# Optimization experiments

Measured on AMD Instinct MI355X. Metric: run time of the kernel, lower is better.

## Reference

```python
import jax, jax.numpy as jnp
import numpy as np
from jax import lax

B, H, L, DK = 8, 8, 1024, 64
BN_EPS = 1e-5


def _conv_bn_sm(x, w, b, g, beta, pad):
    # x: [B, H, L] (N=batch, C=h heads as channels, spatial=L)
    y = lax.conv_general_dilated(x, w, (1,), [(pad, pad)], dimension_numbers=("NCH", "OIH", "NCH"))
    y = y + b[None, :, None]
    # BatchNorm1d in training mode: batch stats over (N, L) per channel, biased var
    mu = jnp.mean(y, axis=(0, 2), keepdims=True)
    var = jnp.var(y, axis=(0, 2), keepdims=True)
    y = (y - mu) * (g[None, :, None] / jnp.sqrt(var + BN_EPS)) + beta[None, :, None]
    return jax.nn.softmax(y, axis=-1)


def setup_inputs() -> dict:
    key = jax.random.key(0)
    ks = jax.random.split(key, 20)
    n = lambda i, shape, s=1.0: jax.random.normal(ks[i], shape, dtype=jnp.float32) * s
    inp = {
        "Q": n(0, (B, H, L, DK)),
        "K": n(1, (B, H, L, DK)),
        "V": n(2, (B, H, L, DK)),
        "attn_mask": jnp.ones((1,), dtype=bool),
        # proj_q / proj_k: Linear(d_k, 1, bias=False) weight [1, d_k] -> stored as [d_k]
        "wq": n(3, (DK,), 0.1), "wk": n(4, (DK,), 0.1),
        # proj_back_q / proj_back_k: Linear(1, d_k, bias=False) weight [d_k, 1] -> [d_k]
        "wbq": n(5, (DK,), 0.1), "wbk": n(6, (DK,), 0.1),
        # Conv1d(h, h, f) weights [out=h, in=h, f] + bias [h]
        "cq3_w": n(7, (H, H, 3), 0.2), "cq3_b": n(8, (H,), 0.05),
        "cq9_w": n(9, (H, H, 9), 0.1), "cq9_b": n(10, (H,), 0.05),
        "ck3_w": n(11, (H, H, 3), 0.2), "ck3_b": n(12, (H,), 0.05),
        "ck9_w": n(13, (H, H, 9), 0.1), "ck9_b": n(14, (H,), 0.05),
        # BatchNorm1d affine params
        "bnq3_g": jnp.ones((H,), jnp.float32), "bnq3_b": jnp.zeros((H,), jnp.float32),
        "bnq9_g": jnp.ones((H,), jnp.float32), "bnq9_b": jnp.zeros((H,), jnp.float32),
        "bnk3_g": jnp.ones((H,), jnp.float32), "bnk3_b": jnp.zeros((H,), jnp.float32),
        "bnk9_g": jnp.ones((H,), jnp.float32), "bnk9_b": jnp.zeros((H,), jnp.float32),
    }
    return inp


def reference(Q, K, V, attn_mask, wq, wk, wbq, wbk,
              cq3_w, cq3_b, cq9_w, cq9_b, ck3_w, ck3_b, ck9_w, ck9_b,
              bnq3_g, bnq3_b, bnq9_g, bnq9_b, bnk3_g, bnk3_b, bnk9_g, bnk9_b):
    b, h, l, d_k = Q.shape
    l_k = K.shape[2]
    # proj to scalar per position, reshape to [b, h, l]
    Qp = jnp.einsum("bhld,d->bhl", Q, wq)
    Kp = jnp.einsum("bhld,d->bhl", K, wk)
    # multi-scale conv + BN(train) + softmax branches
    q0 = _conv_bn_sm(Qp, cq3_w, cq3_b, bnq3_g, bnq3_b, 1)
    q1 = _conv_bn_sm(Qp, cq9_w, cq9_b, bnq9_g, bnq9_b, 4)
    k0 = _conv_bn_sm(Kp, ck3_w, ck3_b, bnk3_g, bnk3_b, 1)
    k1 = _conv_bn_sm(Kp, ck9_w, ck9_b, bnk9_g, bnk9_b, 4)
    # faithful to torch: cat along dim 0 then C-order reshape to [b,h,l,2], max over last
    Qm = jnp.max(jnp.concatenate([q0, q1], axis=0).reshape(b, h, l, 2), axis=-1)
    Km = jnp.max(jnp.concatenate([k0, k1], axis=0).reshape(b, h, l_k, 2), axis=-1)
    # proj back 1 -> d_k (no bias): outer with weight vector
    Qn = Qm[..., None] * wbq  # [b,h,l,d_k]
    Kn = Km[..., None] * wbk  # [b,h,l_k,d_k]
    scores = jnp.einsum("bhqd,bhkd->bhqk", Qn, Kn) / jnp.sqrt(jnp.float32(d_k))
    attn = jax.nn.softmax(scores, axis=-1)
    context = jnp.einsum("bhqk,bhkd->bhqd", attn, V)
    return (context, attn)
```

## Files before the change

kernel.cpp:

```cpp
#include <hip/hip_runtime.h>

constexpr int SL = 1024;
constexpr int NBH = 64;

constexpr int QP_OFF = 0;
constexpr int KP_OFF = 65536;
constexpr int Y_OFF  = 131072;
constexpr int P_OFF  = 393216;
constexpr int QM_OFF = 655360;
constexpr int KM_OFF = 720896;
constexpr int ST_OFF = 786432;
constexpr int C_OFF  = 786496;
constexpr int VT_OFF = 786560;

typedef __attribute__((ext_vector_type(8))) short short8;
typedef __attribute__((ext_vector_type(4))) float f32x4;

__device__ inline unsigned short f2bf(float x) {
    unsigned int u = __float_as_uint(x);
    unsigned int r = (u + 0x7fff + ((u >> 16) & 1)) >> 16;
    return (unsigned short)r;
}

__global__ __launch_bounds__(256) void k_proj(
    const float* __restrict__ Q, const float* __restrict__ K,
    const float* __restrict__ wq, const float* __restrict__ wk,
    const float* __restrict__ wbq, const float* __restrict__ wbk,
    float* __restrict__ ws)
{
    int wid  = (blockIdx.x * 256 + threadIdx.x) >> 6;
    int lane = threadIdx.x & 63;
    const int nrows = 2 * NBH * SL;
    if (wid < nrows) {
        bool isQ = wid < NBH * SL;
        int row = isQ ? wid : wid - NBH * SL;
        const float* src = isQ ? Q : K;
        const float* w   = isQ ? wq : wk;
        float v = src[row * 64 + lane] * w[lane];
        #pragma unroll
        for (int m = 32; m; m >>= 1) v += __shfl_xor(v, m);
        if (lane == 0) ws[(isQ ? QP_OFF : KP_OFF) + row] = v;
    } else if (wid == nrows) {
        float v = wbq[lane] * wbk[lane];
        #pragma unroll
        for (int m = 32; m; m >>= 1) v += __shfl_xor(v, m);
        if (lane == 0) ws[C_OFF] = v * 0.125f;
    }
}

__global__ __launch_bounds__(256) void k_conv(
    float* __restrict__ ws,
    const float* __restrict__ w0, const float* __restrict__ b0,
    const float* __restrict__ w1, const float* __restrict__ b1,
    const float* __restrict__ w2, const float* __restrict__ b2,
    const float* __restrict__ w3, const float* __restrict__ b3)
{
    int branch = blockIdx.x >> 6;
    int n = (blockIdx.x >> 3) & 7;
    int seg = blockIdx.x & 7;
    int t0 = seg * 128;
    const float* wp = branch == 0 ? w0 : branch == 1 ? w1 : branch == 2 ? w2 : w3;
    const float* bp = branch == 0 ? b0 : branch == 1 ? b1 : branch == 2 ? b2 : b3;
    const int F = (branch & 1) ? 9 : 3;
    const int PAD = F >> 1;
    const float* x = ws + ((branch < 2) ? QP_OFF : KP_OFF) + n * 8 * SL;

    __shared__ float xl[8][136];
    __shared__ float wl[8 * 8 * 9];
    __shared__ float bl[8];
    int tid = threadIdx.x;
    for (int i = tid; i < 8 * 8 * F; i += 256) wl[i] = wp[i];
    if (tid < 8) bl[tid] = bp[tid];
    for (int i = tid; i < 8 * 136; i += 256) {
        int ci = i >> 7;
        ci = i / 136; int tt = i - ci * 136;
        int ta = t0 + tt - 4;
        xl[ci][tt] = (ta >= 0 && ta < SL) ? x[ci * SL + ta] : 0.f;
    }
    __syncthreads();
    int c = tid >> 5, u = tid & 31;
    float s1 = 0.f, s2 = 0.f;
    float* yout = ws + Y_OFF + branch * (NBH * SL) + (n * 8 + c) * SL + t0;
    float res[4];
    #pragma unroll
    for (int q = 0; q < 4; q++) {
        int tl = u * 4 + q;
        float acc = bl[c];
        for (int ci = 0; ci < 8; ci++) {
            const float* xr = &xl[ci][tl + 4 - PAD];
            const float* wr = &wl[(c * 8 + ci) * F];
            for (int f = 0; f < F; f++) acc += wr[f] * xr[f];
        }
        res[q] = acc;
        s1 += acc; s2 += acc * acc;
    }
    *(float4*)&yout[u * 4] = make_float4(res[0], res[1], res[2], res[3]);
    #pragma unroll
    for (int m = 16; m; m >>= 1) {
        s1 += __shfl_xor(s1, m);
        s2 += __shfl_xor(s2, m);
    }
    if (u == 0) {
        atomicAdd(&ws[ST_OFF + (branch * 8 + c) * 2],     s1);
        atomicAdd(&ws[ST_OFF + (branch * 8 + c) * 2 + 1], s2);
    }
}

__global__ __launch_bounds__(256) void k_bnsm(
    float* __restrict__ ws,
    const float* __restrict__ g0, const float* __restrict__ be0,
    const float* __restrict__ g1, const float* __restrict__ be1,
    const float* __restrict__ g2, const float* __restrict__ be2,
    const float* __restrict__ g3, const float* __restrict__ be3)
{
    int row = blockIdx.x;
    int branch = row >> 6, n = (row >> 3) & 7, c = row & 7;
    const float* gp = branch == 0 ? g0 : branch == 1 ? g1 : branch == 2 ? g2 : g3;
    const float* bp = branch == 0 ? be0 : branch == 1 ? be1 : branch == 2 ? be2 : be3;
    float s1 = ws[ST_OFF + (branch * 8 + c) * 2];
    float s2 = ws[ST_OFF + (branch * 8 + c) * 2 + 1];
    float mu  = s1 * (1.f / 8192.f);
    float var = s2 * (1.f / 8192.f) - mu * mu;
    float sc = gp[c] * rsqrtf(var + 1e-5f);
    float sh = bp[c] - mu * sc;
    const float* y = ws + Y_OFF + branch * (NBH * SL) + (n * 8 + c) * SL;
    float* p       = ws + P_OFF + branch * (NBH * SL) + (n * 8 + c) * SL;
    int tid = threadIdx.x;
    float4 yv = ((const float4*)y)[tid];
    float z0 = yv.x * sc + sh, z1 = yv.y * sc + sh, z2 = yv.z * sc + sh, z3 = yv.w * sc + sh;
    float mx = fmaxf(fmaxf(z0, z1), fmaxf(z2, z3));
    __shared__ float r1[4], r2[4];
    #pragma unroll
    for (int m = 32; m; m >>= 1) mx = fmaxf(mx, __shfl_xor(mx, m));
    if ((tid & 63) == 0) r1[tid >> 6] = mx;
    __syncthreads();
    mx = fmaxf(fmaxf(r1[0], r1[1]), fmaxf(r1[2], r1[3]));
    float e0 = __expf(z0 - mx), e1 = __expf(z1 - mx), e2 = __expf(z2 - mx), e3 = __expf(z3 - mx);
    float s = e0 + e1 + e2 + e3;
    #pragma unroll
    for (int m = 32; m; m >>= 1) s += __shfl_xor(s, m);
    if ((tid & 63) == 0) r2[tid >> 6] = s;
    __syncthreads();
    s = r2[0] + r2[1] + r2[2] + r2[3];
    float r = 1.f / s;
    ((float4*)p)[tid] = make_float4(e0 * r, e1 * r, e2 * r, e3 * r);
}

__global__ __launch_bounds__(256) void k_mix(float* __restrict__ ws)
{
    int idx = blockIdx.x * 256 + threadIdx.x;
    int which = idx >> 16;
    int r = idx & 65535;
    int i = r >> 13, j = (r >> 10) & 7, k = r & 1023;
    int n  = 2 * i + (j >= 4 ? 1 : 0);
    int br = which * 2 + (n >= 8 ? 1 : 0);
    int row = n & 7;
    int jp  = 2 * (j & 3) + (k >= 512 ? 1 : 0);
    int k2  = (2 * k) & 1023;
    const float* src = ws + P_OFF + br * (NBH * SL) + (row * 8 + jp) * SL;
    float v = fmaxf(src[k2], src[k2 + 1]);
    ws[(which ? KM_OFF : QM_OFF) + r] = v;
}

__global__ __launch_bounds__(256) void k_vpack(const float* __restrict__ V, float* __restrict__ ws)
{
    int t = blockIdx.x * 256 + threadIdx.x;
    int lane = t & 63;
    int s    = (t >> 6) & 7;
    int dsub = (t >> 9) & 3;
    int chunk= (t >> 11) & 3;
    int bh   = t >> 13;
    const float* vb = V + bh * (SL * 64);
    int k0 = chunk * 256 + s * 32 + (lane >> 4) * 8;
    int d  = dsub * 16 + (lane & 15);
    unsigned short o[8];
    #pragma unroll
    for (int j = 0; j < 8; j++) o[j] = f2bf(vb[(k0 + j) * 64 + d]);
    unsigned short* vt = (unsigned short*)(ws + VT_OFF);
    *(short8*)(vt + (size_t)t * 8) = *(short8*)o;
}

__global__ __launch_bounds__(256) void k_attn(
    float* __restrict__ out, const float* __restrict__ ws)
{
    int bh = blockIdx.x >> 4;
    int qt = blockIdx.x & 15;
    int tid = threadIdx.x;
    __shared__ float kml[1024];
    __shared__ float aq[64], mq[64], rq[64];
    __shared__ unsigned short bpk[4 * 8 * 64 * 8];
    __shared__ float red[256];
    __shared__ float rmx[4], rmn[4];

    const float* km = ws + KM_OFF + bh * SL;
    const float* qm = ws + QM_OFF + bh * SL + qt * 64;
    float c = ws[C_OFF];

    float lmax = -1e30f, lmin = 1e30f;
    #pragma unroll
    for (int i = 0; i < 4; i++) {
        float v = km[tid + 256 * i];
        kml[tid + 256 * i] = v;
        lmax = fmaxf(lmax, v); lmin = fminf(lmin, v);
    }
    #pragma unroll
    for (int m = 32; m; m >>= 1) {
        lmax = fmaxf(lmax, __shfl_xor(lmax, m));
        lmin = fminf(lmin, __shfl_xor(lmin, m));
    }
    if ((tid & 63) == 0) { rmx[tid >> 6] = lmax; rmn[tid >> 6] = lmin; }
    __syncthreads();
    float kmax = fmaxf(fmaxf(rmx[0], rmx[1]), fmaxf(rmx[2], rmx[3]));
    float kmin = fminf(fminf(rmn[0], rmn[1]), fminf(rmn[2], rmn[3]));
    if (tid < 64) {
        float a = c * qm[tid];
        aq[tid] = a;
        mq[tid] = (a > 0.f) ? a * kmax : a * kmin;
    }
    __syncthreads();
    {
        int q = tid >> 2, g = tid & 3;
        float a = aq[q], m = mq[q];
        float s = 0.f;
        const float* kp = kml + g * 256;
        for (int k = 0; k < 256; k++) s += __expf(a * kp[k] - m);
        red[tid] = s;
        __syncthreads();
        if (tid < 64) {
            float d = red[tid * 4] + red[tid * 4 + 1] + red[tid * 4 + 2] + red[tid * 4 + 3];
            rq[tid] = 1.f / d;
        }
        __syncthreads();
    }

    int w = tid >> 6, lane = tid & 63;
    int m16 = lane & 15, kg = lane >> 4;
    int qloc = w * 16 + m16;
    float a = aq[qloc], mm = mq[qloc], rr = rq[qloc];
    float* attn_row = out + 4194304 + ((size_t)(bh * SL + qt * 64 + qloc)) * SL;
    const uint4* vt4 = (const uint4*)((const unsigned short*)(ws + VT_OFF) + (size_t)bh * 4 * 16384);

    f32x4 acc0 = {0,0,0,0}, acc1 = {0,0,0,0}, acc2 = {0,0,0,0}, acc3 = {0,0,0,0};

    for (int ch = 0; ch < 4; ch++) {
        const uint4* src = vt4 + ch * 2048;
        uint4* dst = (uint4*)bpk;
        #pragma unroll
        for (int i = 0; i < 8; i++) dst[tid + 256 * i] = src[tid + 256 * i];
        __syncthreads();

        #pragma unroll
        for (int s = 0; s < 8; s++) {
            int k0 = ch * 256 + s * 32 + kg * 8;
            const float* kp = kml + k0;
            float e[8];
            #pragma unroll
            for (int j = 0; j < 8; j++) e[j] = __expf(a * kp[j] - mm) * rr;
            *(float4*)(attn_row + k0)     = make_float4(e[0], e[1], e[2], e[3]);
            *(float4*)(attn_row + k0 + 4) = make_float4(e[4], e[5], e[6], e[7]);
            unsigned short af[8];
            #pragma unroll
            for (int j = 0; j < 8; j++) af[j] = f2bf(e[j]);
            short8 av = *(short8*)af;
            const short8* bbase = (const short8*)bpk + s * 64 + lane;
            short8 b0 = bbase[0 * 512];
            short8 b1 = bbase[1 * 512];
            short8 b2 = bbase[2 * 512];
            short8 b3 = bbase[3 * 512];
            acc0 = __builtin_amdgcn_mfma_f32_16x16x32_bf16(av, b0, acc0, 0, 0, 0);
            acc1 = __builtin_amdgcn_mfma_f32_16x16x32_bf16(av, b1, acc1, 0, 0, 0);
            acc2 = __builtin_amdgcn_mfma_f32_16x16x32_bf16(av, b2, acc2, 0, 0, 0);
            acc3 = __builtin_amdgcn_mfma_f32_16x16x32_bf16(av, b3, acc3, 0, 0, 0);
        }
        __syncthreads();
    }
    float* ctx = out + ((size_t)(bh * SL + qt * 64 + w * 16)) * 64;
    #pragma unroll
    for (int reg = 0; reg < 4; reg++) {
        int row = kg * 4 + reg;
        float* cp = ctx + row * 64 + m16;
        cp[0]  = acc0[reg];
        cp[16] = acc1[reg];
        cp[32] = acc2[reg];
        cp[48] = acc3[reg];
    }
}

extern "C" void kernel_launch(void* const* d_in, const int* in_sizes, int n_in,
                              void* d_out, int out_size, void* d_ws, size_t ws_size,
                              hipStream_t stream)
{
    const float* Q      = (const float*)d_in[0];
    const float* K      = (const float*)d_in[1];
    const float* V      = (const float*)d_in[2];
    const float* wq     = (const float*)d_in[4];
    const float* wk     = (const float*)d_in[5];
    const float* wbq    = (const float*)d_in[6];
    const float* wbk    = (const float*)d_in[7];
    const float* cq3_w  = (const float*)d_in[8];
    const float* cq3_b  = (const float*)d_in[9];
    const float* cq9_w  = (const float*)d_in[10];
    const float* cq9_b  = (const float*)d_in[11];
    const float* ck3_w  = (const float*)d_in[12];
    const float* ck3_b  = (const float*)d_in[13];
    const float* ck9_w  = (const float*)d_in[14];
    const float* ck9_b  = (const float*)d_in[15];
    const float* bnq3_g = (const float*)d_in[16];
    const float* bnq3_b = (const float*)d_in[17];
    const float* bnq9_g = (const float*)d_in[18];
    const float* bnq9_b = (const float*)d_in[19];
    const float* bnk3_g = (const float*)d_in[20];
    const float* bnk3_b = (const float*)d_in[21];
    const float* bnk9_g = (const float*)d_in[22];
    const float* bnk9_b = (const float*)d_in[23];
    float* out = (float*)d_out;
    float* ws  = (float*)d_ws;

    hipMemsetAsync(ws + ST_OFF, 0, 64 * sizeof(float), stream);

    k_proj<<<32769, 256, 0, stream>>>(Q, K, wq, wk, wbq, wbk, ws);
    k_vpack<<<2048, 256, 0, stream>>>(V, ws);
    k_conv<<<256, 256, 0, stream>>>(ws, cq3_w, cq3_b, cq9_w, cq9_b,
                                    ck3_w, ck3_b, ck9_w, ck9_b);
    k_bnsm<<<256, 256, 0, stream>>>(ws, bnq3_g, bnq3_b, bnq9_g, bnq9_b,
                                    bnk3_g, bnk3_b, bnk9_g, bnk9_b);
    k_mix<<<512, 256, 0, stream>>>(ws);
    k_attn<<<1024, 256, 0, stream>>>(out, ws);
}
```

Before: 426.4 us.

## Fuse projection with V pack, BN-softmax with mix, stream V from global in attention

Merges the Q/K projection and V bf16 packing into one launch, with the projection now using float4 loads over 16 lanes per row. Fuses the BN+softmax kernel with the max-mix kernel so the intermediate softmax buffer is never written. In the attention kernel, V fragments are read directly from global memory instead of being staged through LDS with barriers, and attention probabilities are written with nontemporal stores. This cuts launches, intermediate traffic and syncs, but gives up LDS reuse of V across waves.

Result: slower. 451.2 us (+5.8%).

```diff
diff --git a/kernel.cpp b/kernel.cpp
--- a/kernel.cpp
+++ b/kernel.cpp
@@ -6,7 +6,6 @@
 constexpr int QP_OFF = 0;
 constexpr int KP_OFF = 65536;
 constexpr int Y_OFF  = 131072;
-constexpr int P_OFF  = 393216;
 constexpr int QM_OFF = 655360;
 constexpr int KM_OFF = 720896;
 constexpr int ST_OFF = 786432;
@@ -22,29 +21,49 @@
     return (unsigned short)r;
 }
 
-__global__ __launch_bounds__(256) void k_proj(
+__global__ __launch_bounds__(256) void k_projpack(
     const float* __restrict__ Q, const float* __restrict__ K,
+    const float* __restrict__ V,
     const float* __restrict__ wq, const float* __restrict__ wk,
     const float* __restrict__ wbq, const float* __restrict__ wbk,
     float* __restrict__ ws)
 {
-    int wid  = (blockIdx.x * 256 + threadIdx.x) >> 6;
-    int lane = threadIdx.x & 63;
-    const int nrows = 2 * NBH * SL;
-    if (wid < nrows) {
-        bool isQ = wid < NBH * SL;
-        int row = isQ ? wid : wid - NBH * SL;
+    int b = blockIdx.x;
+    int tid = threadIdx.x;
+    if (b < 8192) {
+        bool isQ = b < 4096;
         const float* src = isQ ? Q : K;
         const float* w   = isQ ? wq : wk;
-        float v = src[row * 64 + lane] * w[lane];
+        int row = (b - (isQ ? 0 : 4096)) * 16 + (tid >> 4);
+        int l16 = tid & 15;
+        float4 x  = ((const float4*)(src + row * 64))[l16];
+        float4 w4 = ((const float4*)w)[l16];
+        float v = x.x * w4.x + x.y * w4.y + x.z * w4.z + x.w * w4.w;
         #pragma unroll
-        for (int m = 32; m; m >>= 1) v += __shfl_xor(v, m);
-        if (lane == 0) ws[(isQ ? QP_OFF : KP_OFF) + row] = v;
-    } else if (wid == nrows) {
-        float v = wbq[lane] * wbk[lane];
+        for (int m = 8; m; m >>= 1) v += __shfl_xor(v, m);
+        if (l16 == 0) ws[(isQ ? QP_OFF : KP_OFF) + row] = v;
+    } else if (b < 10240) {
+        int t = (b - 8192) * 256 + tid;
+        int lane = t & 63;
+        int s    = (t >> 6) & 7;
+        int dsub = (t >> 9) & 3;
+        int chunk= (t >> 11) & 3;
+        int bh   = t >> 13;
+        const float* vb = V + bh * (SL * 64);
+        int k0 = chunk * 256 + s * 32 + (lane >> 4) * 8;
+        int d  = dsub * 16 + (lane & 15);
+        unsigned short o[8];
         #pragma unroll
-        for (int m = 32; m; m >>= 1) v += __shfl_xor(v, m);
-        if (lane == 0) ws[C_OFF] = v * 0.125f;
+        for (int j = 0; j < 8; j++) o[j] = f2bf(vb[(k0 + j) * 64 + d]);
+        unsigned short* vt = (unsigned short*)(ws + VT_OFF);
+        *(short8*)(vt + (size_t)t * 8) = *(short8*)o;
+    } else {
+        if (tid < 64) {
+            float v = wbq[tid] * wbk[tid];
+            #pragma unroll
+            for (int m = 32; m; m >>= 1) v += __shfl_xor(v, m);
+            if (tid == 0) ws[C_OFF] = v * 0.125f;
+        }
     }
 }
 
@@ -72,8 +91,7 @@
     for (int i = tid; i < 8 * 8 * F; i += 256) wl[i] = wp[i];
     if (tid < 8) bl[tid] = bp[tid];
     for (int i = tid; i < 8 * 136; i += 256) {
-        int ci = i >> 7;
-        ci = i / 136; int tt = i - ci * 136;
+        int ci = i / 136; int tt = i - ci * 136;
         int ta = t0 + tt - 4;
         xl[ci][tt] = (ta >= 0 && ta < SL) ? x[ci * SL + ta] : 0.f;
     }
@@ -106,78 +124,59 @@
     }
 }
 
-__global__ __launch_bounds__(256) void k_bnsm(
+__global__ __launch_bounds__(256) void k_bnmix(
     float* __restrict__ ws,
     const float* __restrict__ g0, const float* __restrict__ be0,
     const float* __restrict__ g1, const float* __restrict__ be1,
     const float* __restrict__ g2, const float* __restrict__ be2,
     const float* __restrict__ g3, const float* __restrict__ be3)
 {
-    int row = blockIdx.x;
-    int branch = row >> 6, n = (row >> 3) & 7, c = row & 7;
-    const float* gp = branch == 0 ? g0 : branch == 1 ? g1 : branch == 2 ? g2 : g3;
-    const float* bp = branch == 0 ? be0 : branch == 1 ? be1 : branch == 2 ? be2 : be3;
-    float s1 = ws[ST_OFF + (branch * 8 + c) * 2];
-    float s2 = ws[ST_OFF + (branch * 8 + c) * 2 + 1];
+    int blk = blockIdx.x;
+    int which = blk >> 6;
+    int i = (blk >> 3) & 7, j = blk & 7;
+    int n = 2 * i + (j >= 4 ? 1 : 0);
+    int br = which * 2 + (n >= 8 ? 1 : 0);
+    int row = n & 7;
+    int tid = threadIdx.x;
+    int half = tid >> 7;
+    int u = tid & 127;
+    int c = 2 * (j & 3) + half;
+    const float* gp = br == 0 ? g0 : br == 1 ? g1 : br == 2 ? g2 : g3;
+    const float* bp = br == 0 ? be0 : br == 1 ? be1 : br == 2 ? be2 : be3;
+    float s1 = ws[ST_OFF + (br * 8 + c) * 2];
+    float s2 = ws[ST_OFF + (br * 8 + c) * 2 + 1];
     float mu  = s1 * (1.f / 8192.f);
     float var = s2 * (1.f / 8192.f) - mu * mu;
     float sc = gp[c] * rsqrtf(var + 1e-5f);
     float sh = bp[c] - mu * sc;
-    const float* y = ws + Y_OFF + branch * (NBH * SL) + (n * 8 + c) * SL;
-    float* p       = ws + P_OFF + branch * (NBH * SL) + (n * 8 + c) * SL;
-    int tid = threadIdx.x;
-    float4 yv = ((const float4*)y)[tid];
-    float z0 = yv.x * sc + sh, z1 = yv.y * sc + sh, z2 = yv.z * sc + sh, z3 = yv.w * sc + sh;
-    float mx = fmaxf(fmaxf(z0, z1), fmaxf(z2, z3));
+    const float* y = ws + Y_OFF + br * (NBH * SL) + (row * 8 + c) * SL;
+    float4 ya = ((const float4*)y)[u * 2];
+    float4 yb = ((const float4*)y)[u * 2 + 1];
+    float z[8] = { ya.x * sc + sh, ya.y * sc + sh, ya.z * sc + sh, ya.w * sc + sh,
+                   yb.x * sc + sh, yb.y * sc + sh, yb.z * sc + sh, yb.w * sc + sh };
+    float mx = z[0];
+    #pragma unroll
+    for (int q = 1; q < 8; q++) mx = fmaxf(mx, z[q]);
     __shared__ float r1[4], r2[4];
     #pragma unroll
     for (int m = 32; m; m >>= 1) mx = fmaxf(mx, __shfl_xor(mx, m));
     if ((tid & 63) == 0) r1[tid >> 6] = mx;
     __syncthreads();
-    mx = fmaxf(fmaxf(r1[0], r1[1]), fmaxf(r1[2], r1[3]));
-    float e0 = __expf(z0 - mx), e1 = __expf(z1 - mx), e2 = __expf(z2 - mx), e3 = __expf(z3 - mx);
-    float s = e0 + e1 + e2 + e3;
+    mx = half ? fmaxf(r1[2], r1[3]) : fmaxf(r1[0], r1[1]);
+    float e[8];
+    float s = 0.f;
+    #pragma unroll
+    for (int q = 0; q < 8; q++) { e[q] = __expf(z[q] - mx); s += e[q]; }
     #pragma unroll
     for (int m = 32; m; m >>= 1) s += __shfl_xor(s, m);
     if ((tid & 63) == 0) r2[tid >> 6] = s;
     __syncthreads();
-    s = r2[0] + r2[1] + r2[2] + r2[3];
-    float r = 1.f / s;
-    ((float4*)p)[tid] = make_float4(e0 * r, e1 * r, e2 * r, e3 * r);
-}
-
-__global__ __launch_bounds__(256) void k_mix(float* __restrict__ ws)
-{
-    int idx = blockIdx.x * 256 + threadIdx.x;
-    int which = idx >> 16;
-    int r = idx & 65535;
-    int i = r >> 13, j = (r >> 10) & 7, k = r & 1023;
-    int n  = 2 * i + (j >= 4 ? 1 : 0);
-    int br = which * 2 + (n >= 8 ? 1 : 0);
-    int row = n & 7;
-    int jp  = 2 * (j & 3) + (k >= 512 ? 1 : 0);
-    int k2  = (2 * k) & 1023;
-    const float* src = ws + P_OFF + br * (NBH * SL) + (row * 8 + jp) * SL;
-    float v = fmaxf(src[k2], src[k2 + 1]);
-    ws[(which ? KM_OFF : QM_OFF) + r] = v;
-}
-
-__global__ __launch_bounds__(256) void k_vpack(const float* __restrict__ V, float* __restrict__ ws)
-{
-    int t = blockIdx.x * 256 + threadIdx.x;
-    int lane = t & 63;
-    int s    = (t >> 6) & 7;
-    int dsub = (t >> 9) & 3;
-    int chunk= (t >> 11) & 3;
-    int bh   = t >> 13;
-    const float* vb = V + bh * (SL * 64);
-    int k0 = chunk * 256 + s * 32 + (lane >> 4) * 8;
-    int d  = dsub * 16 + (lane & 15);
-    unsigned short o[8];
-    #pragma unroll
-    for (int j = 0; j < 8; j++) o[j] = f2bf(vb[(k0 + j) * 64 + d]);
-    unsigned short* vt = (unsigned short*)(ws + VT_OFF);
-    *(short8*)(vt + (size_t)t * 8) = *(short8*)o;
+    s = half ? (r2[2] + r2[3]) : (r2[0] + r2[1]);
+    float inv = 1.f / s;
+    float4 o = make_float4(fmaxf(e[0], e[1]) * inv, fmaxf(e[2], e[3]) * inv,
+                           fmaxf(e[4], e[5]) * inv, fmaxf(e[6], e[7]) * inv);
+    float* outp = ws + (which ? KM_OFF : QM_OFF) + i * 8192 + j * 1024 + half * 512;
+    ((float4*)outp)[u] = o;
 }
 
 __global__ __launch_bounds__(256) void k_attn(
@@ -188,7 +187,6 @@
     int tid = threadIdx.x;
     __shared__ float kml[1024];
     __shared__ float aq[64], mq[64], rq[64];
-    __shared__ unsigned short bpk[4 * 8 * 64 * 8];
     __shared__ float red[256];
     __shared__ float rmx[4], rmn[4];
 
@@ -238,41 +236,34 @@
     int qloc = w * 16 + m16;
     float a = aq[qloc], mm = mq[qloc], rr = rq[qloc];
     float* attn_row = out + 4194304 + ((size_t)(bh * SL + qt * 64 + qloc)) * SL;
-    const uint4* vt4 = (const uint4*)((const unsigned short*)(ws + VT_OFF) + (size_t)bh * 4 * 16384);
+    const short8* vb = (const short8*)((const unsigned short*)(ws + VT_OFF)) + (size_t)bh * 8192;
 
     f32x4 acc0 = {0,0,0,0}, acc1 = {0,0,0,0}, acc2 = {0,0,0,0}, acc3 = {0,0,0,0};
 
-    for (int ch = 0; ch < 4; ch++) {
-        const uint4* src = vt4 + ch * 2048;
-        uint4* dst = (uint4*)bpk;
+    for (int s = 0; s < 32; s++) {
+        int ch = s >> 3, ks = s & 7;
+        const short8* bbase = vb + ch * 2048 + ks * 64 + lane;
+        short8 b0 = bbase[0];
+        short8 b1 = bbase[512];
+        short8 b2 = bbase[1024];
+        short8 b3 = bbase[1536];
+        int k0 = s * 32 + kg * 8;
+        const float* kp = kml + k0;
+        float e[8];
         #pragma unroll
-        for (int i = 0; i < 8; i++) dst[tid + 256 * i] = src[tid + 256 * i];
-        __syncthreads();
-
+        for (int j = 0; j < 8; j++) e[j] = __expf(a * kp[j] - mm) * rr;
+        f32x4 e0123 = { e[0], e[1], e[2], e[3] };
+        f32x4 e4567 = { e[4], e[5], e[6], e[7] };
+        __builtin_nontemporal_store(e0123, (f32x4*)(attn_row + k0));
+        __builtin_nontemporal_store(e4567, (f32x4*)(attn_row + k0 + 4));
+        unsigned short af[8];
         #pragma unroll
-        for (int s = 0; s < 8; s++) {
-            int k0 = ch * 256 + s * 32 + kg * 8;
-            const float* kp = kml + k0;
-            float e[8];
-            #pragma unroll
-            for (int j = 0; j < 8; j++) e[j] = __expf(a * kp[j] - mm) * rr;
-            *(float4*)(attn_row + k0)     = make_float4(e[0], e[1], e[2], e[3]);
-            *(float4*)(attn_row + k0 + 4) = make_float4(e[4], e[5], e[6], e[7]);
-            unsigned short af[8];
-            #pragma unroll
-            for (int j = 0; j < 8; j++) af[j] = f2bf(e[j]);
-            short8 av = *(short8*)af;
-            const short8* bbase = (const short8*)bpk + s * 64 + lane;
-            short8 b0 = bbase[0 * 512];
-            short8 b1 = bbase[1 * 512];
-            short8 b2 = bbase[2 * 512];
-            short8 b3 = bbase[3 * 512];
-            acc0 = __builtin_amdgcn_mfma_f32_16x16x32_bf16(av, b0, acc0, 0, 0, 0);
-            acc1 = __builtin_amdgcn_mfma_f32_16x16x32_bf16(av, b1, acc1, 0, 0, 0);
-            acc2 = __builtin_amdgcn_mfma_f32_16x16x32_bf16(av, b2, acc2, 0, 0, 0);
-            acc3 = __builtin_amdgcn_mfma_f32_16x16x32_bf16(av, b3, acc3, 0, 0, 0);
-        }
-        __syncthreads();
+        for (int j = 0; j < 8; j++) af[j] = f2bf(e[j]);
+        short8 av = *(short8*)af;
+        acc0 = __builtin_amdgcn_mfma_f32_16x16x32_bf16(av, b0, acc0, 0, 0, 0);
+        acc1 = __builtin_amdgcn_mfma_f32_16x16x32_bf16(av, b1, acc1, 0, 0, 0);
+        acc2 = __builtin_amdgcn_mfma_f32_16x16x32_bf16(av, b2, acc2, 0, 0, 0);
+        acc3 = __builtin_amdgcn_mfma_f32_16x16x32_bf16(av, b3, acc3, 0, 0, 0);
     }
     float* ctx = out + ((size_t)(bh * SL + qt * 64 + w * 16)) * 64;
     #pragma unroll
@@ -316,14 +307,12 @@
     float* out = (float*)d_out;
     float* ws  = (float*)d_ws;
 
-    hipMemsetAsync(ws + ST_OFF, 0, 64 * sizeof(float), stream);
-
-    k_proj<<<32769, 256, 0, stream>>>(Q, K, wq, wk, wbq, wbk, ws);
-    k_vpack<<<2048, 256, 0, stream>>>(V, ws);
+    (void)hipMemsetAsync(ws + ST_OFF, 0, 64 * sizeof(float), stream);
+
+    k_projpack<<<10241, 256, 0, stream>>>(Q, K, V, wq, wk, wbq, wbk, ws);
     k_conv<<<256, 256, 0, stream>>>(ws, cq3_w, cq3_b, cq9_w, cq9_b,
                                     ck3_w, ck3_b, ck9_w, ck9_b);
-    k_bnsm<<<256, 256, 0, stream>>>(ws, bnq3_g, bnq3_b, bnq9_g, bnq9_b,
-                                    bnk3_g, bnk3_b, bnk9_g, bnk9_b);
-    k_mix<<<512, 256, 0, stream>>>(ws);
+    k_bnmix<<<128, 256, 0, stream>>>(ws, bnq3_g, bnq3_b, bnq9_g, bnq9_b,
+                                     bnk3_g, bnk3_b, bnk9_g, bnk9_b);
     k_attn<<<1024, 256, 0, stream>>>(out, ws);
 }
```
